# Kernel optimization log

Hardware: AMD Instinct MI355X
Metric: run time of the kernel (lower is better)

## Reference

```python
import jax, jax.numpy as jnp
import numpy as np

D_IN, D_H, D_OUT = 1024, 1024, 1024
D_MOE = 4096
N_EXPERTS = 8
TOP_K = 2


def setup_inputs() -> dict:
    key = jax.random.key(0)
    ks = jax.random.split(key, 10)
    s = lambda d: 1.0 / np.sqrt(d)
    x = jax.random.normal(ks[0], (2, 2048, D_IN), dtype=jnp.float32)
    W_in = jax.random.normal(ks[1], (D_IN, D_H), dtype=jnp.float32) * s(D_IN)
    b_in = jnp.zeros((D_H,), jnp.float32)
    W_gate = jax.random.normal(ks[2], (D_H, N_EXPERTS), dtype=jnp.float32) * s(D_H)
    b_gate = jnp.zeros((N_EXPERTS,), jnp.float32)
    W1 = jax.random.normal(ks[3], (N_EXPERTS, D_H, D_MOE), dtype=jnp.float32) * s(D_H)
    b1 = jnp.zeros((N_EXPERTS, D_MOE), jnp.float32)
    W2 = jax.random.normal(ks[4], (N_EXPERTS, D_MOE, D_H), dtype=jnp.float32) * s(D_MOE)
    b2 = jnp.zeros((N_EXPERTS, D_H), jnp.float32)
    W_out = jax.random.normal(ks[5], (D_H, D_OUT), dtype=jnp.float32) * s(D_H)
    b_out = jnp.zeros((D_OUT,), jnp.float32)
    return {"x": x, "W_in": W_in, "b_in": b_in, "W_gate": W_gate, "b_gate": b_gate,
            "W1": W1, "b1": b1, "W2": W2, "b2": b2, "W_out": W_out, "b_out": b_out}


def reference(x, W_in, b_in, W_gate, b_gate, W1, b1, W2, b2, W_out, b_out):
    B, S, _ = x.shape
    h = x @ W_in + b_in                       # [B,S,D_H]
    t = h.reshape(B * S, -1)                  # tokens [N,D_H]

    # --- top-k softmax gating ---
    logits = t @ W_gate + b_gate              # [N,E]
    probs = jax.nn.softmax(logits, axis=-1)
    topv, topi = jax.lax.top_k(probs, TOP_K)  # [N,k]
    topv = topv / jnp.sum(topv, axis=-1, keepdims=True)
    # dense routing weights [N,E] (zeros for unselected experts)
    route = jnp.zeros_like(probs).at[jnp.arange(t.shape[0])[:, None], topi].set(topv)

    # --- expert MLPs (dense all-expert compute, weighted combine) ---
    mid = jax.nn.relu(jnp.einsum('nd,edh->neh', t, W1) + b1)   # [N,E,D_MOE]
    eout = jnp.einsum('neh,ehd->ned', mid, W2) + b2            # [N,E,D_H]
    moe_out = jnp.einsum('ne,ned->nd', route, eout)            # [N,D_H]

    out = moe_out.reshape(B, S, -1) @ W_out + b_out            # [B,S,D_OUT]
    return out
```

## Files before the change

kernel.cpp:

```cpp
#include <hip/hip_runtime.h>
#include <hip/hip_bf16.h>

typedef __bf16 bf16_t;
typedef bf16_t bf16x8 __attribute__((ext_vector_type(8)));
typedef bf16_t bf16x4 __attribute__((ext_vector_type(4)));
typedef float f32x4 __attribute__((ext_vector_type(4)));

#define DIN 1024
#define DH 1024
#define DMOE 4096
#define NEXP 8
#define NTOK 4096

__device__ __forceinline__ void gload_lds16(const bf16_t* g, bf16_t* l) {
  __builtin_amdgcn_global_load_lds(
      (const __attribute__((address_space(1))) void*)g,
      (__attribute__((address_space(3))) void*)l, 16, 0, 0);
}


__global__ void k_zero8(int* p) {
  if (threadIdx.x < 8) p[threadIdx.x] = 0;
}

__global__ void k_transpose_cvt(const float* __restrict__ src, bf16_t* __restrict__ dst,
                                int R, int C) {
  __shared__ float tile[64][65];
  const size_t mofs = (size_t)blockIdx.z * R * C;
  const float* s = src + mofs;
  bf16_t* d = dst + mofs;
  const int c0 = blockIdx.x * 64, r0 = blockIdx.y * 64;
  const int t = threadIdx.x;
  const int rr = t >> 4;
  const int cc = (t & 15) << 2;
#pragma unroll
  for (int i = 0; i < 64; i += 16) {
    const float4 v = *(const float4*)&s[(size_t)(r0 + rr + i) * C + c0 + cc];
    tile[rr + i][cc + 0] = v.x;
    tile[rr + i][cc + 1] = v.y;
    tile[rr + i][cc + 2] = v.z;
    tile[rr + i][cc + 3] = v.w;
  }
  __syncthreads();
  const int orr = (t & 7) * 8;
  const int oc = t >> 3;
#pragma unroll
  for (int i = 0; i < 64; i += 32) {
    bf16x8 o;
#pragma unroll
    for (int j = 0; j < 8; ++j) o[j] = (bf16_t)tile[orr + j][oc + i];
    *(bf16x8*)&d[(size_t)(c0 + oc + i) * R + r0 + orr] = o;
  }
}

__global__ void k_cvt_bf16(const float* __restrict__ src, bf16_t* __restrict__ dst, int n4) {
  const int i = blockIdx.x * blockDim.x + threadIdx.x;
  if (i < n4) {
    const float4 v = *(const float4*)(src + (size_t)i * 4);
    bf16x4 o;
    o.x = (bf16_t)v.x; o.y = (bf16_t)v.y; o.z = (bf16_t)v.z; o.w = (bf16_t)v.w;
    *(bf16x4*)(dst + (size_t)i * 4) = o;
  }
}

__global__ void k_gate_prep(const float* __restrict__ Win, const float* __restrict__ Wgate,
                            const float* __restrict__ b_in, const float* __restrict__ b_gate,
                            double* __restrict__ G, double* __restrict__ cvec) {
  const int lane = threadIdx.x & 63;
  const int wave = (blockIdx.x * blockDim.x + threadIdx.x) >> 6;
  const int nw = (gridDim.x * blockDim.x) >> 6;
  for (int d = wave; d <= DIN; d += nw) {
    const float* row = (d < DIN) ? (Win + (size_t)d * DH) : b_in;
    double acc[8] = {0, 0, 0, 0, 0, 0, 0, 0};
    for (int k = lane; k < DH; k += 64) {
      const double xv = (double)row[k];
      const float* g = Wgate + (size_t)k * NEXP;
#pragma unroll
      for (int ee = 0; ee < 8; ++ee) acc[ee] += xv * (double)g[ee];
    }
#pragma unroll
    for (int ee = 0; ee < 8; ++ee) {
      double a = acc[ee];
      for (int o = 32; o > 0; o >>= 1) a += __shfl_down(a, o);
      acc[ee] = a;
    }
    if (lane == 0) {
      if (d < DIN) {
#pragma unroll
        for (int ee = 0; ee < 8; ++ee) G[(size_t)d * 8 + ee] = acc[ee];
      } else {
#pragma unroll
        for (int ee = 0; ee < 8; ++ee) cvec[ee] = acc[ee] + (double)b_gate[ee];
      }
    }
  }
}

__global__ void k_gating(const float* __restrict__ x, const double* __restrict__ G,
                         const double* __restrict__ cvec, int* __restrict__ cnt,
                         int* __restrict__ list, float* __restrict__ wlist) {
  const int lane = threadIdx.x & 63;
  const int t = blockIdx.x * (blockDim.x >> 6) + (threadIdx.x >> 6);
  if (t >= NTOK) return;
  const float* xr = x + (size_t)t * DIN;
  double acc[8] = {0, 0, 0, 0, 0, 0, 0, 0};
  for (int d = lane; d < DIN; d += 64) {
    const double xv = (double)xr[d];
    const double* g = G + (size_t)d * 8;
#pragma unroll
    for (int ee = 0; ee < 8; ++ee) acc[ee] += xv * g[ee];
  }
#pragma unroll
  for (int ee = 0; ee < 8; ++ee) {
    double a = acc[ee];
    for (int o = 32; o > 0; o >>= 1) a += __shfl_down(a, o);
    acc[ee] = a;
  }
  if (lane == 0) {
    double l[8];
#pragma unroll
    for (int ee = 0; ee < 8; ++ee) l[ee] = acc[ee] + cvec[ee];
    double m = l[0];
#pragma unroll
    for (int ee = 1; ee < 8; ++ee) m = fmax(m, l[ee]);
    double p[8];
#pragma unroll
    for (int ee = 0; ee < 8; ++ee) p[ee] = exp(l[ee] - m);
    int i1 = 0;
#pragma unroll
    for (int ee = 1; ee < 8; ++ee)
      if (p[ee] > p[i1]) i1 = ee;
    int i2 = (i1 == 0) ? 1 : 0;
#pragma unroll
    for (int ee = 0; ee < 8; ++ee)
      if (ee != i1 && p[ee] > p[i2]) i2 = ee;
    const double s2 = p[i1] + p[i2];
    const float w1 = (float)(p[i1] / s2);
    const float w2 = (float)(p[i2] / s2);
    int lp = atomicAdd(&cnt[i1], 1);
    list[i1 * NTOK + lp] = t * 2;
    wlist[i1 * NTOK + lp] = w1;
    lp = atomicAdd(&cnt[i2], 1);
    list[i2 * NTOK + lp] = t * 2 + 1;
    wlist[i2 * NTOK + lp] = w2;
  }
}

__global__ void k_scan(const int* __restrict__ cnt, int* __restrict__ offs) {
  if (threadIdx.x == 0) {
    int s = 0;
    for (int e = 0; e < NEXP; ++e) { offs[e] = s; s += cnt[e]; }
    offs[NEXP] = s;
  }
}

__global__ void k_combine(const bf16_t* __restrict__ eout, bf16_t* __restrict__ moebf) {
  const int i = blockIdx.x * blockDim.x + threadIdx.x;
  const int t = i >> 8;
  const int q = (i & 255) * 4;
  const bf16x4 a = *(const bf16x4*)(eout + ((size_t)t * 2) * DH + q);
  const bf16x4 b = *(const bf16x4*)(eout + ((size_t)t * 2 + 1) * DH + q);
  bf16x4 o;
  o.x = (bf16_t)((float)a.x + (float)b.x);
  o.y = (bf16_t)((float)a.y + (float)b.y);
  o.z = (bf16_t)((float)a.z + (float)b.z);
  o.w = (bf16_t)((float)a.w + (float)b.w);
  *(bf16x4*)(moebf + (size_t)t * DH + q) = o;
}

template <int MODE>
__global__ __launch_bounds__(256, 3) void k_gemm(
    const bf16_t* __restrict__ Abase, const bf16_t* __restrict__ Bbase,
    const float* __restrict__ biasBase, void* __restrict__ Cbase,
    int M, int N, int K,
    const int* __restrict__ cnt, const int* __restrict__ offs,
    const int* __restrict__ listBase, const float* __restrict__ wlistBase) {
  const int e = blockIdx.z;
  const int mblk = blockIdx.y, nblk = blockIdx.x;
  int Mloc = M;
  const bf16_t* A = Abase;
  const bf16_t* B = Bbase;
  const float* bias = biasBase;
  const int* myList = nullptr;
  const float* myW = nullptr;
  int rowOff = 0;
  if constexpr (MODE == 1 || MODE == 2) {
    Mloc = cnt[e];
    if (mblk * 128 >= Mloc) return;
    B = Bbase + (size_t)e * N * K;
    bias = biasBase + (size_t)e * N;
    myList = listBase + e * NTOK;
    myW = wlistBase + e * NTOK;
    rowOff = offs[e];
    if constexpr (MODE == 2) A = Abase + (size_t)rowOff * K;
  }

  __shared__ bf16_t As[3][128 * 32];
  __shared__ bf16_t Bs[3][128 * 32];

  const int tid = threadIdx.x;
  const int lane = tid & 63;
  const int wid = tid >> 6;
  const int wr = wid >> 1, wc = wid & 1;

  const int srow0 = wid * 32 + (lane >> 2);
  const int srow1 = srow0 + 16;
  const int skcol = ((lane & 3) ^ ((lane >> 3) & 3)) * 8;

  int ar0 = mblk * 128 + srow0;
  int ar1 = mblk * 128 + srow1;
  if constexpr (MODE == 1 || MODE == 2) {
    if (ar0 > Mloc - 1) ar0 = Mloc - 1;
    if (ar1 > Mloc - 1) ar1 = Mloc - 1;
  }
  size_t arow0 = (size_t)ar0, arow1 = (size_t)ar1;
  if constexpr (MODE == 1) {
    arow0 = (size_t)(myList[ar0] >> 1);
    arow1 = (size_t)(myList[ar1] >> 1);
  }
  const bf16_t* aptr0 = A + arow0 * K + skcol;
  const bf16_t* aptr1 = A + arow1 * K + skcol;
  const bf16_t* bptr0 = B + (size_t)(nblk * 128 + srow0) * K + skcol;
  const bf16_t* bptr1 = B + (size_t)(nblk * 128 + srow1) * K + skcol;

  const int ldsOfsA0 = (wid * 32) * 32;
  const int ldsOfsA1 = (wid * 32 + 16) * 32;

  f32x4 acc[4][4] = {};

  const int nkt = K >> 5;

  auto stage = [&](int buf, int kt) {
    const size_t ko = (size_t)kt * 32;
    gload_lds16(aptr0 + ko, &As[buf][ldsOfsA0]);
    gload_lds16(aptr1 + ko, &As[buf][ldsOfsA1]);
    gload_lds16(bptr0 + ko, &Bs[buf][ldsOfsA0]);
    gload_lds16(bptr1 + ko, &Bs[buf][ldsOfsA1]);
  };

  stage(0, 0);
  if (nkt > 1) stage(1, 1);

  const int fr = lane & 15;
  const int s0 = (((lane >> 4) ^ ((fr >> 1) & 3)) << 3);

  int cur = 0;
  for (int kt = 0; kt < nkt; ++kt) {
    int nxt = cur + 2;
    if (nxt >= 3) nxt -= 3;
    if (kt + 2 < nkt) {
      stage(nxt, kt + 2);
      asm volatile("s_waitcnt vmcnt(8)" ::: "memory");
    } else if (kt + 1 < nkt) {
      asm volatile("s_waitcnt vmcnt(4)" ::: "memory");
    } else {
      asm volatile("s_waitcnt vmcnt(0)" ::: "memory");
    }
    __builtin_amdgcn_s_barrier();

    bf16x8 af[4], bfr[4];
#pragma unroll
    for (int m = 0; m < 4; ++m)
      af[m] = *(const bf16x8*)&As[cur][(wr * 64 + m * 16 + fr) * 32 + s0];
#pragma unroll
    for (int n = 0; n < 4; ++n)
      bfr[n] = *(const bf16x8*)&Bs[cur][(wc * 64 + n * 16 + fr) * 32 + s0];
#pragma unroll
    for (int m = 0; m < 4; ++m)
#pragma unroll
      for (int n = 0; n < 4; ++n)
        acc[m][n] = __builtin_amdgcn_mfma_f32_16x16x32_bf16(af[m], bfr[n], acc[m][n], 0, 0, 0);

    __builtin_amdgcn_s_barrier();
    cur += 1;
    if (cur >= 3) cur -= 3;
  }

  const int colBase = nblk * 128 + wc * 64 + (lane & 15);
  const int rowBase = mblk * 128 + wr * 64 + ((lane >> 4) << 2);
#pragma unroll
  for (int n = 0; n < 4; ++n) {
    const int c = colBase + n * 16;
    const float bv = bias[c];
#pragma unroll
    for (int m = 0; m < 4; ++m) {
#pragma unroll
      for (int j = 0; j < 4; ++j) {
        const int r = rowBase + m * 16 + j;
        float v = acc[m][n][j] + bv;
        if constexpr (MODE == 0) {
          ((bf16_t*)Cbase)[(size_t)r * N + c] = (bf16_t)v;
        } else if constexpr (MODE == 1) {
          if (r < Mloc) {
            v = fmaxf(v, 0.0f);
            ((bf16_t*)Cbase)[(size_t)(rowOff + r) * N + c] = (bf16_t)v;
          }
        } else if constexpr (MODE == 2) {
          if (r < Mloc) {
            const int entry = myList[r];
            const float w = myW[r];
            ((bf16_t*)Cbase)[(size_t)entry * DH + c] = (bf16_t)(v * w);
          }
        } else {
          ((float*)Cbase)[(size_t)r * N + c] = v;
        }
      }
    }
  }
}


extern "C" void kernel_launch(void* const* d_in, const int* in_sizes, int n_in,
                              void* d_out, int out_size, void* d_ws, size_t ws_size,
                              hipStream_t stream) {
  const float* x      = (const float*)d_in[0];
  const float* W_in   = (const float*)d_in[1];
  const float* b_in   = (const float*)d_in[2];
  const float* W_gate = (const float*)d_in[3];
  const float* b_gate = (const float*)d_in[4];
  const float* W1     = (const float*)d_in[5];
  const float* b1     = (const float*)d_in[6];
  const float* W2     = (const float*)d_in[7];
  const float* b2     = (const float*)d_in[8];
  const float* W_out  = (const float*)d_in[9];
  const float* b_out  = (const float*)d_in[10];

  char* ws = (char*)d_ws;
  size_t off = 0;
  auto alloc = [&](size_t bytes) -> void* {
    void* p = ws + off;
    off += (bytes + 255) & ~(size_t)255;
    return p;
  };

  bf16_t* WtIn  = (bf16_t*)alloc((size_t)DH * DIN * 2);
  bf16_t* Wt1   = (bf16_t*)alloc((size_t)NEXP * DMOE * DH * 2);
  bf16_t* Wt2   = (bf16_t*)alloc((size_t)NEXP * DH * DMOE * 2);
  bf16_t* WtOut = (bf16_t*)alloc((size_t)DH * DH * 2);
  bf16_t* xbf   = (bf16_t*)alloc((size_t)NTOK * DIN * 2);
  bf16_t* hbf   = (bf16_t*)alloc((size_t)NTOK * DH * 2);
  bf16_t* mid   = (bf16_t*)alloc((size_t)2 * NTOK * DMOE * 2);
  bf16_t* eoutb = (bf16_t*)alloc((size_t)2 * NTOK * DH * 2);
  bf16_t* moebf = (bf16_t*)alloc((size_t)NTOK * DH * 2);
  double* G     = (double*)alloc((size_t)DIN * 8 * 8);
  double* cvec  = (double*)alloc(8 * 8);
  int*    cnt   = (int*)alloc(NEXP * 4);
  int*    offs  = (int*)alloc((NEXP + 1) * 4);
  int*    list  = (int*)alloc((size_t)NEXP * NTOK * 4);
  float*  wlist = (float*)alloc((size_t)NEXP * NTOK * 4);

  k_zero8<<<1, 64, 0, stream>>>(cnt);

  k_transpose_cvt<<<dim3(DH / 64, DIN / 64, 1), 256, 0, stream>>>(W_in, WtIn, DIN, DH);
  k_transpose_cvt<<<dim3(DMOE / 64, DH / 64, NEXP), 256, 0, stream>>>(W1, Wt1, DH, DMOE);
  k_transpose_cvt<<<dim3(DH / 64, DMOE / 64, NEXP), 256, 0, stream>>>(W2, Wt2, DMOE, DH);
  k_transpose_cvt<<<dim3(DH / 64, DH / 64, 1), 256, 0, stream>>>(W_out, WtOut, DH, DH);
  k_cvt_bf16<<<(NTOK * DIN / 4 + 255) / 256, 256, 0, stream>>>(x, xbf, NTOK * DIN / 4);

  k_gate_prep<<<64, 256, 0, stream>>>(W_in, W_gate, b_in, b_gate, G, cvec);
  k_gating<<<NTOK / 4, 256, 0, stream>>>(x, G, cvec, cnt, list, wlist);
  k_scan<<<1, 64, 0, stream>>>(cnt, offs);

  k_gemm<0><<<dim3(DH / 128, NTOK / 128, 1), 256, 0, stream>>>(
      xbf, WtIn, b_in, hbf, NTOK, DH, DIN, nullptr, nullptr, nullptr, nullptr);
  k_gemm<1><<<dim3(DMOE / 128, NTOK / 128, NEXP), 256, 0, stream>>>(
      hbf, Wt1, b1, mid, NTOK, DMOE, DH, cnt, offs, list, wlist);
  k_gemm<2><<<dim3(DH / 128, NTOK / 128, NEXP), 256, 0, stream>>>(
      mid, Wt2, b2, eoutb, NTOK, DH, DMOE, cnt, offs, list, wlist);
  k_combine<<<NTOK * DH / 4 / 256, 256, 0, stream>>>(eoutb, moebf);
  k_gemm<3><<<dim3(DH / 128, NTOK / 128, 1), 256, 0, stream>>>(
      moebf, WtOut, b_out, (float*)d_out, NTOK, DH, DH, nullptr, nullptr, nullptr, nullptr);
}
```

Baseline: 570.1 us.

## Fuse weight transposes into one launch and use 256-row tiles for expert GEMM1

Merges the four weight transpose/convert launches into one flat-grid kernel and folds the counter zeroing into the gate-prep kernel, removing several launches. Adds a dedicated 512-thread expert up-projection GEMM with 256x128 tiles, gathering token rows through the routing list with 32-bit offsets. Each B tile is now reused across twice as many rows. In exchange, LDS use and thread count per block go up, and experts with few tokens waste more of each tile.

```diff
diff --git a/kernel.cpp b/kernel.cpp
--- a/kernel.cpp
+++ b/kernel.cpp
@@ -18,18 +18,28 @@
       (__attribute__((address_space(3))) void*)l, 16, 0, 0);
 }
 
-
-__global__ void k_zero8(int* p) {
-  if (threadIdx.x < 8) p[threadIdx.x] = 0;
-}
-
-__global__ void k_transpose_cvt(const float* __restrict__ src, bf16_t* __restrict__ dst,
-                                int R, int C) {
+__global__ void k_transpose_all(const float* __restrict__ W_in, const float* __restrict__ W1,
+                                const float* __restrict__ W2, const float* __restrict__ W_out,
+                                bf16_t* __restrict__ WtIn, bf16_t* __restrict__ Wt1,
+                                bf16_t* __restrict__ Wt2, bf16_t* __restrict__ WtOut) {
+  const int z = blockIdx.x;
+  const float* s; bf16_t* d; int R, C, tx, ty;
+  if (z < 256) {
+    s = W_in; d = WtIn; R = DIN; C = DH; tx = z & 15; ty = z >> 4;
+  } else if (z < 8448) {
+    const int l = z - 256, e = l >> 10, t = l & 1023;
+    s = W1 + (size_t)e * DH * DMOE; d = Wt1 + (size_t)e * DH * DMOE;
+    R = DH; C = DMOE; tx = t & 63; ty = t >> 6;
+  } else if (z < 16640) {
+    const int l = z - 8448, e = l >> 10, t = l & 1023;
+    s = W2 + (size_t)e * DMOE * DH; d = Wt2 + (size_t)e * DMOE * DH;
+    R = DMOE; C = DH; tx = t & 15; ty = t >> 4;
+  } else {
+    const int t = z - 16640;
+    s = W_out; d = WtOut; R = DH; C = DH; tx = t & 15; ty = t >> 4;
+  }
   __shared__ float tile[64][65];
-  const size_t mofs = (size_t)blockIdx.z * R * C;
-  const float* s = src + mofs;
-  bf16_t* d = dst + mofs;
-  const int c0 = blockIdx.x * 64, r0 = blockIdx.y * 64;
+  const int c0 = tx * 64, r0 = ty * 64;
   const int t = threadIdx.x;
   const int rr = t >> 4;
   const int cc = (t & 15) << 2;
@@ -65,7 +75,9 @@
 
 __global__ void k_gate_prep(const float* __restrict__ Win, const float* __restrict__ Wgate,
                             const float* __restrict__ b_in, const float* __restrict__ b_gate,
-                            double* __restrict__ G, double* __restrict__ cvec) {
+                            double* __restrict__ G, double* __restrict__ cvec,
+                            int* __restrict__ cnt) {
+  if (blockIdx.x == 0 && threadIdx.x < 8) cnt[threadIdx.x] = 0;
   const int lane = threadIdx.x & 63;
   const int wave = (blockIdx.x * blockDim.x + threadIdx.x) >> 6;
   const int nw = (gridDim.x * blockDim.x) >> 6;
@@ -183,16 +195,14 @@
   const float* bias = biasBase;
   const int* myList = nullptr;
   const float* myW = nullptr;
-  int rowOff = 0;
-  if constexpr (MODE == 1 || MODE == 2) {
+  if constexpr (MODE == 2) {
     Mloc = cnt[e];
     if (mblk * 128 >= Mloc) return;
     B = Bbase + (size_t)e * N * K;
     bias = biasBase + (size_t)e * N;
     myList = listBase + e * NTOK;
     myW = wlistBase + e * NTOK;
-    rowOff = offs[e];
-    if constexpr (MODE == 2) A = Abase + (size_t)rowOff * K;
+    A = Abase + (size_t)offs[e] * K;
   }
 
   __shared__ bf16_t As[3][128 * 32];
@@ -209,17 +219,12 @@
 
   int ar0 = mblk * 128 + srow0;
   int ar1 = mblk * 128 + srow1;
-  if constexpr (MODE == 1 || MODE == 2) {
+  if constexpr (MODE == 2) {
     if (ar0 > Mloc - 1) ar0 = Mloc - 1;
     if (ar1 > Mloc - 1) ar1 = Mloc - 1;
   }
-  size_t arow0 = (size_t)ar0, arow1 = (size_t)ar1;
-  if constexpr (MODE == 1) {
-    arow0 = (size_t)(myList[ar0] >> 1);
-    arow1 = (size_t)(myList[ar1] >> 1);
-  }
-  const bf16_t* aptr0 = A + arow0 * K + skcol;
-  const bf16_t* aptr1 = A + arow1 * K + skcol;
+  const bf16_t* aptr0 = A + (size_t)ar0 * K + skcol;
+  const bf16_t* aptr1 = A + (size_t)ar1 * K + skcol;
   const bf16_t* bptr0 = B + (size_t)(nblk * 128 + srow0) * K + skcol;
   const bf16_t* bptr1 = B + (size_t)(nblk * 128 + srow1) * K + skcol;
 
@@ -227,7 +232,6 @@
   const int ldsOfsA1 = (wid * 32 + 16) * 32;
 
   f32x4 acc[4][4] = {};
-
   const int nkt = K >> 5;
 
   auto stage = [&](int buf, int kt) {
@@ -290,11 +294,6 @@
         float v = acc[m][n][j] + bv;
         if constexpr (MODE == 0) {
           ((bf16_t*)Cbase)[(size_t)r * N + c] = (bf16_t)v;
-        } else if constexpr (MODE == 1) {
-          if (r < Mloc) {
-            v = fmaxf(v, 0.0f);
-            ((bf16_t*)Cbase)[(size_t)(rowOff + r) * N + c] = (bf16_t)v;
-          }
         } else if constexpr (MODE == 2) {
           if (r < Mloc) {
             const int entry = myList[r];
@@ -303,6 +302,109 @@
           }
         } else {
           ((float*)Cbase)[(size_t)r * N + c] = v;
+        }
+      }
+    }
+  }
+}
+
+__global__ __launch_bounds__(512, 4) void k_gemm1(
+    const bf16_t* __restrict__ Abase, const bf16_t* __restrict__ Bbase,
+    const float* __restrict__ biasBase, bf16_t* __restrict__ Cbase,
+    int N, int K,
+    const int* __restrict__ cnt, const int* __restrict__ offs,
+    const int* __restrict__ listBase) {
+  const int e = blockIdx.z;
+  const int mblk = blockIdx.y, nblk = blockIdx.x;
+  const int Mloc = cnt[e];
+  if (mblk * 256 >= Mloc) return;
+  const bf16_t* B = Bbase + (size_t)e * N * K;
+  const float* bias = biasBase + (size_t)e * N;
+  const int* myList = listBase + e * NTOK;
+  const int rowOff = offs[e];
+
+  __shared__ bf16_t As[3][256 * 32];
+  __shared__ bf16_t Bs[3][128 * 32];
+
+  const int tid = threadIdx.x;
+  const int lane = tid & 63;
+  const int wid = tid >> 6;
+  const int wr = wid >> 1, wc = wid & 1;
+
+  const int subr = lane >> 2;
+  const int skcol = ((lane & 3) ^ ((lane >> 3) & 3)) * 8;
+
+  uint32_t aofs[2];
+#pragma unroll
+  for (int l = 0; l < 2; ++l) {
+    int ar = mblk * 256 + (wid * 2 + l) * 16 + subr;
+    if (ar > Mloc - 1) ar = Mloc - 1;
+    aofs[l] = (uint32_t)(myList[ar] >> 1) * (uint32_t)K + skcol;
+  }
+  const uint32_t bofs = (uint32_t)(nblk * 128 + wid * 16 + subr) * (uint32_t)K + skcol;
+
+  f32x4 acc[4][4] = {};
+  const int nkt = K >> 5;
+
+  auto stage = [&](int buf, int kt) {
+    const uint32_t ko = (uint32_t)kt * 32;
+    gload_lds16(Abase + aofs[0] + ko, &As[buf][(wid * 2 + 0) * 512]);
+    gload_lds16(Abase + aofs[1] + ko, &As[buf][(wid * 2 + 1) * 512]);
+    gload_lds16(B + bofs + ko, &Bs[buf][wid * 512]);
+  };
+
+  stage(0, 0);
+  if (nkt > 1) stage(1, 1);
+
+  const int fr = lane & 15;
+  const int s0 = (((lane >> 4) ^ ((fr >> 1) & 3)) << 3);
+
+  int cur = 0;
+  for (int kt = 0; kt < nkt; ++kt) {
+    int nxt = cur + 2;
+    if (nxt >= 3) nxt -= 3;
+    if (kt + 2 < nkt) {
+      stage(nxt, kt + 2);
+      asm volatile("s_waitcnt vmcnt(6)" ::: "memory");
+    } else if (kt + 1 < nkt) {
+      asm volatile("s_waitcnt vmcnt(3)" ::: "memory");
+    } else {
+      asm volatile("s_waitcnt vmcnt(0)" ::: "memory");
+    }
+    __builtin_amdgcn_s_barrier();
+
+    bf16x8 af[4], bfr[4];
+#pragma unroll
+    for (int m = 0; m < 4; ++m)
+      af[m] = *(const bf16x8*)&As[cur][(wr * 64 + m * 16 + fr) * 32 + s0];
+#pragma unroll
+    for (int n = 0; n < 4; ++n)
+      bfr[n] = *(const bf16x8*)&Bs[cur][(wc * 64 + n * 16 + fr) * 32 + s0];
+#pragma unroll
+    for (int m = 0; m < 4; ++m)
+#pragma unroll
+      for (int n = 0; n < 4; ++n)
+        acc[m][n] = __builtin_amdgcn_mfma_f32_16x16x32_bf16(af[m], bfr[n], acc[m][n], 0, 0, 0);
+
+    __builtin_amdgcn_s_barrier();
+    cur += 1;
+    if (cur >= 3) cur -= 3;
+  }
+
+  const int colBase = nblk * 128 + wc * 64 + (lane & 15);
+  const int rowBase = mblk * 256 + wr * 64 + ((lane >> 4) << 2);
+#pragma unroll
+  for (int n = 0; n < 4; ++n) {
+    const int c = colBase + n * 16;
+    const float bv = bias[c];
+#pragma unroll
+    for (int m = 0; m < 4; ++m) {
+#pragma unroll
+      for (int j = 0; j < 4; ++j) {
+        const int r = rowBase + m * 16 + j;
+        if (r < Mloc) {
+          float v = fmaxf(acc[m][n][j] + bv, 0.0f);
+          Cbase[(size_t)(rowOff + r) * N + c] = (bf16_t)v;
         }
       }
     }
@@ -349,22 +451,17 @@
   int*    list  = (int*)alloc((size_t)NEXP * NTOK * 4);
   float*  wlist = (float*)alloc((size_t)NEXP * NTOK * 4);
 
-  k_zero8<<<1, 64, 0, stream>>>(cnt);
-
-  k_transpose_cvt<<<dim3(DH / 64, DIN / 64, 1), 256, 0, stream>>>(W_in, WtIn, DIN, DH);
-  k_transpose_cvt<<<dim3(DMOE / 64, DH / 64, NEXP), 256, 0, stream>>>(W1, Wt1, DH, DMOE);
-  k_transpose_cvt<<<dim3(DH / 64, DMOE / 64, NEXP), 256, 0, stream>>>(W2, Wt2, DMOE, DH);
-  k_transpose_cvt<<<dim3(DH / 64, DH / 64, 1), 256, 0, stream>>>(W_out, WtOut, DH, DH);
+  k_transpose_all<<<16896, 256, 0, stream>>>(W_in, W1, W2, W_out, WtIn, Wt1, Wt2, WtOut);
   k_cvt_bf16<<<(NTOK * DIN / 4 + 255) / 256, 256, 0, stream>>>(x, xbf, NTOK * DIN / 4);
 
-  k_gate_prep<<<64, 256, 0, stream>>>(W_in, W_gate, b_in, b_gate, G, cvec);
+  k_gate_prep<<<64, 256, 0, stream>>>(W_in, W_gate, b_in, b_gate, G, cvec, cnt);
   k_gating<<<NTOK / 4, 256, 0, stream>>>(x, G, cvec, cnt, list, wlist);
   k_scan<<<1, 64, 0, stream>>>(cnt, offs);
 
   k_gemm<0><<<dim3(DH / 128, NTOK / 128, 1), 256, 0, stream>>>(
       xbf, WtIn, b_in, hbf, NTOK, DH, DIN, nullptr, nullptr, nullptr, nullptr);
-  k_gemm<1><<<dim3(DMOE / 128, NTOK / 128, NEXP), 256, 0, stream>>>(
-      hbf, Wt1, b1, mid, NTOK, DMOE, DH, cnt, offs, list, wlist);
+  k_gemm1<<<dim3(DMOE / 128, NTOK / 256, NEXP), 512, 0, stream>>>(
+      hbf, Wt1, b1, mid, DMOE, DH, cnt, offs, list);
   k_gemm<2><<<dim3(DH / 128, NTOK / 128, NEXP), 256, 0, stream>>>(
       mid, Wt2, b2, eoutb, NTOK, DH, DMOE, cnt, offs, list, wlist);
   k_combine<<<NTOK * DH / 4 / 256, 256, 0, stream>>>(eoutb, moebf);
```

After: 560.4 us. Within noise of the previous version (-1.7%).
